# Kernel optimization log

Hardware: AMD Instinct MI355X
Metric: run time of the kernel (lower is better)

The kernel has to match this reference:

```python
import jax, jax.numpy as jnp
import numpy as np

B, I_LEN, Q_LEN, H = 256, 256, 64, 512
MID, G, FLAT_OUT = 512, 1, 1024


def setup_inputs() -> dict:
    key = jax.random.key(0)
    ks = jax.random.split(key, 20)
    s = lambda k, sh: jax.random.normal(k, sh, dtype=jnp.float32) * 0.02
    inp = {
        'i_batch': jax.random.normal(ks[0], (B, I_LEN, H), dtype=jnp.float32),
        'q_batch': jax.random.normal(ks[1], (B, Q_LEN, H), dtype=jnp.float32),
        'i_mask': jax.random.bernoulli(ks[2], 0.1, (B, 1, 1, I_LEN)),
        'q_mask': jax.random.bernoulli(ks[3], 0.1, (B, 1, 1, Q_LEN)),
        # l_flatten (applied to i_feat) params
        'lf_w1': s(ks[4], (H, MID)), 'lf_b1': jnp.zeros((MID,), jnp.float32),
        'lf_w2': s(ks[5], (MID, G)), 'lf_b2': jnp.zeros((G,), jnp.float32),
        'lf_wm': s(ks[6], (H * G, FLAT_OUT)), 'lf_bm': jnp.zeros((FLAT_OUT,), jnp.float32),
        # i_flatten (applied to l_feat) params
        'if_w1': s(ks[7], (H, MID)), 'if_b1': jnp.zeros((MID,), jnp.float32),
        'if_w2': s(ks[8], (MID, G)), 'if_b2': jnp.zeros((G,), jnp.float32),
        'if_wm': s(ks[9], (H * G, FLAT_OUT)), 'if_bm': jnp.zeros((FLAT_OUT,), jnp.float32),
        # fh_h: Linear(1024, 512)
        'fh_w': s(ks[10], (FLAT_OUT, 512)), 'fh_b': jnp.zeros((512,), jnp.float32),
    }
    return inp


def _qkv_attention(query, key, value, mask):
    # query [B,Lq,H], key/value [B,Lk,H], mask [B,1,1,Lk] (True = pad)
    d_k = query.shape[-1]
    scores = jnp.einsum('bqh,bkh->bqk', query, key) / jnp.sqrt(jnp.asarray(d_k, query.dtype))
    scores = jnp.where(mask[:, 0], jnp.asarray(-65504.0, scores.dtype), scores)
    p_attn = jax.nn.softmax(scores, axis=-1)
    return jnp.einsum('bqk,bkh->bqh', p_attn, value)


def _att_flat(x, x_mask, w1, b1, w2, b2, wm, bm):
    # x [B,L,H], x_mask [B,1,1,L]
    att = jnp.maximum(x @ w1 + b1, 0.0) @ w2 + b2           # [B,L,G]
    att = jnp.where(x_mask[:, 0, 0, :, None], -1e9, att)
    att = jax.nn.softmax(att, axis=1)
    pooled = jnp.einsum('blg,blh->bgh', att, x).reshape(x.shape[0], -1)  # [B,G*H]
    return pooled @ wm + bm, att[..., 0]                    # att.squeeze() with G=1


def reference(i_batch, q_batch, i_mask, q_mask,
              lf_w1, lf_b1, lf_w2, lf_b2, lf_wm, lf_bm,
              if_w1, if_b1, if_w2, if_b2, if_wm, if_bm,
              fh_w, fh_b):
    i_feat = _qkv_attention(i_batch, q_batch, q_batch, q_mask)   # [B,I_LEN,H]
    i_feat, i_weight = _att_flat(i_feat, i_mask, lf_w1, lf_b1, lf_w2, lf_b2, lf_wm, lf_bm)
    l_feat = _qkv_attention(q_batch, i_batch, i_batch, i_mask)   # [B,Q_LEN,H]
    l_feat, _ = _att_flat(l_feat, q_mask, if_w1, if_b1, if_w2, if_b2, if_wm, if_bm)
    out = (l_feat + i_feat) @ fh_w + fh_b                        # [B,512]
    return out, i_weight
```

## Files before the change

kernel.cpp:

```cpp
#include <hip/hip_runtime.h>
#include <math.h>


#define SCALE 0.04419417382415922f

typedef __attribute__((ext_vector_type(8))) short short8;
typedef __attribute__((ext_vector_type(4))) float floatx4;

__device__ __forceinline__ unsigned short f2bf(float x) {
  unsigned u = __float_as_uint(x);
  unsigned r = u + 0x7FFFu + ((u >> 16) & 1u);
  return (unsigned short)(r >> 16);
}
__device__ __forceinline__ float bf2f(unsigned short h) {
  return __uint_as_float(((unsigned)h) << 16);
}
__device__ __forceinline__ unsigned pk2(float a, float b) {
  return (unsigned)f2bf(a) | ((unsigned)f2bf(b) << 16);
}

__device__ __forceinline__ float wave_max(float v) {
#pragma unroll
  for (int o = 32; o > 0; o >>= 1) v = fmaxf(v, __shfl_xor(v, o, 64));
  return v;
}
__device__ __forceinline__ float wave_sum(float v) {
#pragma unroll
  for (int o = 32; o > 0; o >>= 1) v += __shfl_xor(v, o, 64);
  return v;
}

#define GLD_LDS16(gptr, lptr)                                             \
  __builtin_amdgcn_global_load_lds(                                       \
      (const __attribute__((address_space(1))) void*)(gptr),              \
      (__attribute__((address_space(3))) void*)(lptr), 16, 0, 0)

__global__ __launch_bounds__(256) void k_prep(
    const float* __restrict__ ib, const float* __restrict__ qb,
    const float* __restrict__ lf_w1, const float* __restrict__ if_w1,
    const float* __restrict__ lf_wm, const float* __restrict__ if_wm,
    const float* __restrict__ fh_w, unsigned short* __restrict__ ibT,
    unsigned short* __restrict__ qb_bf, unsigned short* __restrict__ w1t_lf,
    unsigned short* __restrict__ w1t_if, unsigned short* __restrict__ wcat_t,
    unsigned short* __restrict__ fh_wt) {
  __shared__ __align__(16) char smem[64 * 65 * 4];
  const int idx = blockIdx.x, t = threadIdx.x;

  if (idx < 512) {
    float(*T)[65] = (float(*)[65])smem;
    const float* src;
    unsigned short* dst;
    int N, ds, koff, k0, n0;
    if (idx < 64) {
      src = lf_w1; dst = w1t_lf; N = 512; ds = 512; koff = 0;
      k0 = (idx & 7) * 64; n0 = (idx >> 3) * 64;
    } else if (idx < 128) {
      int l = idx - 64;
      src = if_w1; dst = w1t_if; N = 512; ds = 512; koff = 0;
      k0 = (l & 7) * 64; n0 = (l >> 3) * 64;
    } else if (idx < 256) {
      int l = idx - 128;
      src = lf_wm; dst = wcat_t; N = 1024; ds = 1024; koff = 0;
      k0 = (l & 7) * 64; n0 = (l >> 3) * 64;
    } else if (idx < 384) {
      int l = idx - 256;
      src = if_wm; dst = wcat_t; N = 1024; ds = 1024; koff = 512;
      k0 = (l & 7) * 64; n0 = (l >> 3) * 64;
    } else {
      int l = idx - 384;
      src = fh_w; dst = fh_wt; N = 512; ds = 1024; koff = 0;
      k0 = (l & 15) * 64; n0 = (l >> 4) * 64;
    }
#pragma unroll
    for (int i = 0; i < 16; i++) {
      int e = t + i * 256, r = e >> 6, c = e & 63;
      T[r][c] = src[(size_t)(k0 + r) * N + n0 + c];
    }
    __syncthreads();
#pragma unroll
    for (int i = 0; i < 8; i++) {
      int e = t + i * 256, r = e >> 5, c2 = (e & 31) * 2;
      *(unsigned*)&dst[(size_t)(n0 + r) * ds + koff + k0 + c2] =
          pk2(T[c2][r], T[c2 + 1][r]);
    }
  } else if (idx < 4608) {
    int j = idx - 512;
    int b = j >> 4, tok0 = ((j >> 2) & 3) * 64, h0 = (j & 3) * 128;
    unsigned short* Tb = (unsigned short*)smem;
    const float* src = ib + ((size_t)b * 256 + tok0) * 512 + h0;
#pragma unroll
    for (int i = 0; i < 8; i++) {
      int e = t + i * 256, tok = e >> 5, h4 = (e & 31) * 4;
      float4 v = *(const float4*)&src[(size_t)tok * 512 + h4];
      uint2 p;
      p.x = pk2(v.x, v.y);
      p.y = pk2(v.z, v.w);
      int col = ((((h4 >> 3) ^ (tok >> 3)) & 15) << 3) | (h4 & 7);
      *(uint2*)&Tb[tok * 128 + col] = p;
    }
    __syncthreads();
    unsigned short* dT = ibT + ((size_t)b * 512 + h0) * 256 + tok0;
#pragma unroll
    for (int i = 0; i < 4; i++) {
      int e = t + i * 256, h = e >> 3, tc = (e & 7) * 8;
      int hg = h >> 3, ho = h & 7;
      unsigned y[8];
#pragma unroll
      for (int k = 0; k < 8; k++) {
        int r = tc + k;
        y[k] = Tb[r * 128 + (((hg ^ (r >> 3)) & 15) << 3) + ho];
      }
      uint4 v;
      v.x = y[0] | (y[1] << 16);
      v.y = y[2] | (y[3] << 16);
      v.z = y[4] | (y[5] << 16);
      v.w = y[6] | (y[7] << 16);
      *(uint4*)&dT[(size_t)h * 256 + tc] = v;
    }
  } else {
    int j = idx - 4608;
    const float4* src = (const float4*)(qb + (size_t)j * 4096);
    uint2* dst = (uint2*)(qb_bf + (size_t)j * 4096);
#pragma unroll
    for (int i = 0; i < 4; i++) {
      int e = t + i * 256;
      float4 v = src[e];
      uint2 p;
      p.x = pk2(v.x, v.y);
      p.y = pk2(v.z, v.w);
      dst[e] = p;
    }
  }
}

__global__ __launch_bounds__(256) void k_scores_f(
    const float* __restrict__ ib, const unsigned short* __restrict__ qbf,
    const int* __restrict__ imask, const int* __restrict__ qmask,
    unsigned short* __restrict__ P1, unsigned short* __restrict__ P2,
    float* __restrict__ psum) {
  __shared__ unsigned short As[64 * 64];
  __shared__ unsigned short Bs[128 * 64];
  __shared__ __align__(16) unsigned short X[128 * 72];
  const int b = blockIdx.y, ic = blockIdx.x, i0 = ic * 128;
  const int t = threadIdx.x, w = t >> 6, lane = t & 63, c = lane & 15, qq = lane >> 4;

  floatx4 acc[4][2];
#pragma unroll
  for (int ti = 0; ti < 4; ti++)
#pragma unroll
    for (int tj = 0; tj < 2; tj++) acc[ti][tj] = (floatx4){0.f, 0.f, 0.f, 0.f};

  for (int k0 = 0; k0 < 512; k0 += 64) {
#pragma unroll
    for (int i = 0; i < 2; i++) {
      int s = i * 256 + t, row = s >> 3, src = (s & 7) ^ (row & 7);
      GLD_LDS16(qbf + ((size_t)b * 64 + row) * 512 + k0 + src * 8,
                &As[(i * 256 + w * 64) * 8]);
    }
#pragma unroll
    for (int i = 0; i < 8; i++) {
      int s = i * 256 + t, row = s >> 4, c4 = s & 15;
      float4 v = *(const float4*)&ib[((size_t)b * 256 + i0 + row) * 512 + k0 + c4 * 4];
      int gs = (c4 >> 1) ^ (row & 7), sub = c4 & 1;
      uint2 p;
      p.x = pk2(v.x, v.y);
      p.y = pk2(v.z, v.w);
      *(uint2*)&Bs[row * 64 + gs * 8 + sub * 4] = p;
    }
    __syncthreads();
#pragma unroll
    for (int kk = 0; kk < 2; kk++) {
      short8 a[4], bb[2];
#pragma unroll
      for (int ti = 0; ti < 4; ti++)
        a[ti] = *(const short8*)&As[(ti * 16 + c) * 64 + ((kk * 4 + qq) ^ (c & 7)) * 8];
#pragma unroll
      for (int tj = 0; tj < 2; tj++)
        bb[tj] = *(const short8*)&Bs[(w * 32 + tj * 16 + c) * 64 + ((kk * 4 + qq) ^ (c & 7)) * 8];
#pragma unroll
      for (int ti = 0; ti < 4; ti++)
#pragma unroll
        for (int tj = 0; tj < 2; tj++)
          acc[ti][tj] = __builtin_amdgcn_mfma_f32_16x16x32_bf16(a[ti], bb[tj], acc[ti][tj], 0, 0, 0);
    }
    __syncthreads();
  }

  const int il0 = w * 32 + c;
  int imsk0 = imask[b * 256 + i0 + il0];
  int imsk1 = imask[b * 256 + i0 + il0 + 16];
  int qm[4][4];
#pragma unroll
  for (int ti = 0; ti < 4; ti++)
#pragma unroll
    for (int rr = 0; rr < 4; rr++) qm[ti][rr] = qmask[b * 64 + ti * 16 + qq * 4 + rr];

#pragma unroll
  for (int ti = 0; ti < 4; ti++)
#pragma unroll
    for (int rr = 0; rr < 4; rr++) {
      int qv = ti * 16 + qq * 4 + rr;
      float e0 = imsk0 ? 0.f : __expf(acc[ti][0][rr] * SCALE);
      float e1 = imsk1 ? 0.f : __expf(acc[ti][1][rr] * SCALE);
      X[qv * 136 + il0] = f2bf(e0);
      X[qv * 136 + il0 + 16] = f2bf(e1);
      float s = e0 + e1;
#pragma unroll
      for (int o = 1; o <= 8; o <<= 1) s += __shfl_xor(s, o, 64);
      if (c == 0) psum[((size_t)(b * 64 + qv)) * 8 + ic * 4 + w] = s;
    }
  __syncthreads();
#pragma unroll
  for (int i = 0; i < 4; i++) {
    int e2 = t + i * 256, qv = e2 >> 4, g = e2 & 15;
    *(uint4*)&P2[((size_t)b * 64 + qv) * 256 + i0 + g * 8] = *(const uint4*)&X[qv * 136 + g * 8];
  }
  __syncthreads();

#pragma unroll
  for (int tj = 0; tj < 2; tj++) {
    float ev[4][4];
    float s1 = 0.f;
#pragma unroll
    for (int ti = 0; ti < 4; ti++)
#pragma unroll
      for (int rr = 0; rr < 4; rr++) {
        ev[ti][rr] = qm[ti][rr] ? 0.f : __expf(acc[ti][tj][rr] * SCALE);
        s1 += ev[ti][rr];
      }
    s1 += __shfl_xor(s1, 16, 64);
    s1 += __shfl_xor(s1, 32, 64);
    float inv = 1.f / s1;
    int il = il0 + tj * 16;
#pragma unroll
    for (int ti = 0; ti < 4; ti++)
#pragma unroll
      for (int rr = 0; rr < 4; rr++)
        X[il * 72 + ti * 16 + qq * 4 + rr] = f2bf(ev[ti][rr] * inv);
  }
  __syncthreads();
#pragma unroll
  for (int i = 0; i < 4; i++) {
    int e2 = t + i * 256, il = e2 >> 3, g = e2 & 7;
    *(uint4*)&P1[((size_t)b * 256 + i0 + il) * 64 + g * 8] = *(const uint4*)&X[il * 72 + g * 8];
  }
}

__global__ __launch_bounds__(256) void k_av2(const unsigned short* __restrict__ P2,
                                             const unsigned short* __restrict__ ibT,
                                             const float* __restrict__ psum,
                                             unsigned short* __restrict__ lfeat) {
  __shared__ unsigned short As[64 * 64];
  __shared__ unsigned short Bs[128 * 64];
  const int b = blockIdx.y, n0 = blockIdx.x * 128;
  const int t = threadIdx.x, w = t >> 6, lane = t & 63, c = lane & 15, q = lane >> 4;
  const int wm = w >> 1, wn = w & 1;
  floatx4 acc[2][4];
#pragma unroll
  for (int ti = 0; ti < 2; ti++)
#pragma unroll
    for (int tj = 0; tj < 4; tj++) acc[ti][tj] = (floatx4){0.f, 0.f, 0.f, 0.f};

  for (int kc = 0; kc < 256; kc += 64) {
#pragma unroll
    for (int i = 0; i < 2; i++) {
      int s = i * 256 + t, row = s >> 3, src = (s & 7) ^ (row & 7);
      GLD_LDS16(P2 + ((size_t)b * 64 + row) * 256 + kc + src * 8, &As[(i * 256 + w * 64) * 8]);
    }
#pragma unroll
    for (int i = 0; i < 4; i++) {
      int s = i * 256 + t, row = s >> 3, src = (s & 7) ^ (row & 7);
      GLD_LDS16(ibT + ((size_t)b * 512 + n0 + row) * 256 + kc + src * 8,
                &Bs[(i * 256 + w * 64) * 8]);
    }
    __syncthreads();
#pragma unroll
    for (int kk = 0; kk < 2; kk++) {
      short8 a[2], bb[4];
#pragma unroll
      for (int ti = 0; ti < 2; ti++)
        a[ti] = *(const short8*)&As[(wm * 32 + ti * 16 + c) * 64 + ((kk * 4 + q) ^ (c & 7)) * 8];
#pragma unroll
      for (int tj = 0; tj < 4; tj++)
        bb[tj] = *(const short8*)&Bs[(wn * 64 + tj * 16 + c) * 64 + ((kk * 4 + q) ^ (c & 7)) * 8];
#pragma unroll
      for (int ti = 0; ti < 2; ti++)
#pragma unroll
        for (int tj = 0; tj < 4; tj++)
          acc[ti][tj] = __builtin_amdgcn_mfma_f32_16x16x32_bf16(a[ti], bb[tj], acc[ti][tj], 0, 0, 0);
    }
    __syncthreads();
  }
#pragma unroll
  for (int ti = 0; ti < 2; ti++)
#pragma unroll
    for (int rr = 0; rr < 4; rr++) {
      int m = wm * 32 + ti * 16 + q * 4 + rr;
      const float* ps = psum + ((size_t)(b * 64 + m)) * 8;
      float s = ps[0] + ps[1] + ps[2] + ps[3] + ps[4] + ps[5] + ps[6] + ps[7];
      float inv = 1.f / s;
      unsigned short* op = lfeat + ((size_t)b * 64 + m) * 512 + n0 + wn * 64;
#pragma unroll
      for (int tj = 0; tj < 4; tj++) op[tj * 16 + c] = f2bf(acc[ti][tj][rr] * inv);
    }
}

__global__ __launch_bounds__(256) void k_qbw1(const unsigned short* __restrict__ qbf,
                                              const unsigned short* __restrict__ W1t,
                                              unsigned short* __restrict__ qbW1T) {
  __shared__ unsigned short As[64 * 64];
  __shared__ unsigned short Bs[128 * 64];
  const int b = blockIdx.y, n0 = blockIdx.x * 128;
  const int t = threadIdx.x, w = t >> 6, lane = t & 63, c = lane & 15, q = lane >> 4;
  const int wm = w >> 1, wn = w & 1;
  floatx4 acc[2][4];
#pragma unroll
  for (int ti = 0; ti < 2; ti++)
#pragma unroll
    for (int tj = 0; tj < 4; tj++) acc[ti][tj] = (floatx4){0.f, 0.f, 0.f, 0.f};

  for (int k0 = 0; k0 < 512; k0 += 64) {
#pragma unroll
    for (int i = 0; i < 2; i++) {
      int s = i * 256 + t, row = s >> 3, src = (s & 7) ^ (row & 7);
      GLD_LDS16(qbf + ((size_t)b * 64 + row) * 512 + k0 + src * 8,
                &As[(i * 256 + w * 64) * 8]);
    }
#pragma unroll
    for (int i = 0; i < 4; i++) {
      int s = i * 256 + t, row = s >> 3, src = (s & 7) ^ (row & 7);
      GLD_LDS16(W1t + (size_t)(n0 + row) * 512 + k0 + src * 8,
                &Bs[(i * 256 + w * 64) * 8]);
    }
    __syncthreads();
#pragma unroll
    for (int kk = 0; kk < 2; kk++) {
      short8 a[2], bb[4];
#pragma unroll
      for (int ti = 0; ti < 2; ti++)
        a[ti] = *(const short8*)&As[(wm * 32 + ti * 16 + c) * 64 + ((kk * 4 + q) ^ (c & 7)) * 8];
#pragma unroll
      for (int tj = 0; tj < 4; tj++)
        bb[tj] = *(const short8*)&Bs[(wn * 64 + tj * 16 + c) * 64 + ((kk * 4 + q) ^ (c & 7)) * 8];
#pragma unroll
      for (int ti = 0; ti < 2; ti++)
#pragma unroll
        for (int tj = 0; tj < 4; tj++)
          acc[ti][tj] = __builtin_amdgcn_mfma_f32_16x16x32_bf16(a[ti], bb[tj], acc[ti][tj], 0, 0, 0);
    }
    __syncthreads();
  }
#pragma unroll
  for (int ti = 0; ti < 2; ti++)
#pragma unroll
    for (int tj = 0; tj < 4; tj++) {
      int n = n0 + wn * 64 + tj * 16 + c;
      int m = wm * 32 + ti * 16 + q * 4;
      uint2 p;
      p.x = pk2(acc[ti][tj][0], acc[ti][tj][1]);
      p.y = pk2(acc[ti][tj][2], acc[ti][tj][3]);
      *(uint2*)&qbW1T[((size_t)b * 512 + n) * 64 + m] = p;
    }
}

__global__ __launch_bounds__(256) void k_logits_i64(
    const unsigned short* __restrict__ P1, const unsigned short* __restrict__ qbW1T,
    const float* __restrict__ b1, const float* __restrict__ w2,
    float* __restrict__ outp) {
  __shared__ unsigned short As[128 * 64];
  __shared__ unsigned short Bs[128 * 64];
  __shared__ float red[2][128];
  const int b = blockIdx.y;
  const int mt = blockIdx.x & 1, nc = blockIdx.x >> 1;
  const int m0 = mt * 128, n0 = nc * 128;
  const int t = threadIdx.x, w = t >> 6, lane = t & 63, c = lane & 15, q = lane >> 4;
  const int wm = w >> 1, wn = w & 1;

#pragma unroll
  for (int i = 0; i < 4; i++) {
    int s = i * 256 + t, row = s >> 3, src = (s & 7) ^ (row & 7);
    GLD_LDS16(P1 + ((size_t)b * 256 + m0 + row) * 64 + src * 8, &As[(i * 256 + w * 64) * 8]);
  }
#pragma unroll
  for (int i = 0; i < 4; i++) {
    int s = i * 256 + t, row = s >> 3, src = (s & 7) ^ (row & 7);
    GLD_LDS16(qbW1T + ((size_t)b * 512 + n0 + row) * 64 + src * 8, &Bs[(i * 256 + w * 64) * 8]);
  }
  __syncthreads();
  floatx4 acc[4][4];
#pragma unroll
  for (int ti = 0; ti < 4; ti++)
#pragma unroll
    for (int tj = 0; tj < 4; tj++) acc[ti][tj] = (floatx4){0.f, 0.f, 0.f, 0.f};
#pragma unroll
  for (int kk = 0; kk < 2; kk++) {
    short8 a[4], bb[4];
#pragma unroll
    for (int ti = 0; ti < 4; ti++)
      a[ti] = *(const short8*)&As[(wm * 64 + ti * 16 + c) * 64 + ((kk * 4 + q) ^ (c & 7)) * 8];
#pragma unroll
    for (int tj = 0; tj < 4; tj++)
      bb[tj] = *(const short8*)&Bs[(wn * 64 + tj * 16 + c) * 64 + ((kk * 4 + q) ^ (c & 7)) * 8];
#pragma unroll
    for (int ti = 0; ti < 4; ti++)
#pragma unroll
      for (int tj = 0; tj < 4; tj++)
        acc[ti][tj] = __builtin_amdgcn_mfma_f32_16x16x32_bf16(a[ti], bb[tj], acc[ti][tj], 0, 0, 0);
  }

  float partial[4][4] = {};
#pragma unroll
  for (int tj = 0; tj < 4; tj++) {
    int n = n0 + wn * 64 + tj * 16 + c;
    float bia = b1[n], wwv = w2[n];
#pragma unroll
    for (int ti = 0; ti < 4; ti++)
#pragma unroll
      for (int r = 0; r < 4; r++)
        partial[ti][r] += fmaxf(acc[ti][tj][r] + bia, 0.f) * wwv;
  }
#pragma unroll
  for (int msk = 1; msk <= 8; msk <<= 1)
#pragma unroll
    for (int ti = 0; ti < 4; ti++)
#pragma unroll
      for (int r = 0; r < 4; r++)
        partial[ti][r] += __shfl_xor(partial[ti][r], msk, 64);
  if (c == 0) {
#pragma unroll
    for (int ti = 0; ti < 4; ti++)
#pragma unroll
      for (int r = 0; r < 4; r++)
        red[wn][wm * 64 + ti * 16 + q * 4 + r] = partial[ti][r];
  }
  __syncthreads();
  if (t < 128) outp[(size_t)nc * 65536 + b * 256 + m0 + t] = red[0][t] + red[1][t];
}

__global__ __launch_bounds__(256) void k_logits_part(
    const unsigned short* __restrict__ X, const unsigned short* __restrict__ W1t,
    const float* __restrict__ b1, const float* __restrict__ w2,
    float* __restrict__ outp, int M) {
  __shared__ unsigned short As[128 * 64];
  __shared__ unsigned short Bs[128 * 64];
  __shared__ float red[2][128];
  const int t = threadIdx.x, w = t >> 6, lane = t & 63;
  const int wm = w >> 1, wn = w & 1, c = lane & 15, q = lane >> 4;
  const int idx = blockIdx.x;
  const int m_tile = (idx & 7) + ((idx >> 5) << 3), nc = (idx >> 3) & 3;
  const int m0 = m_tile * 128, n0 = nc * 128;

  floatx4 acc[4][4];
#pragma unroll
  for (int ti = 0; ti < 4; ti++)
#pragma unroll
    for (int tj = 0; tj < 4; tj++) acc[ti][tj] = (floatx4){0.f, 0.f, 0.f, 0.f};

  for (int k0 = 0; k0 < 512; k0 += 64) {
#pragma unroll
    for (int it = 0; it < 4; it++) {
      int s = it * 256 + t, row = s >> 3, src = (s & 7) ^ (row & 7);
      GLD_LDS16(X + (size_t)(m0 + row) * 512 + k0 + src * 8, &As[(it * 256 + w * 64) * 8]);
      GLD_LDS16(W1t + (size_t)(n0 + row) * 512 + k0 + src * 8, &Bs[(it * 256 + w * 64) * 8]);
    }
    __syncthreads();
#pragma unroll
    for (int kk = 0; kk < 2; kk++) {
      short8 a[4], bb[4];
#pragma unroll
      for (int ti = 0; ti < 4; ti++)
        a[ti] = *(const short8*)&As[(wm * 64 + ti * 16 + c) * 64 + ((kk * 4 + q) ^ (c & 7)) * 8];
#pragma unroll
      for (int tj = 0; tj < 4; tj++)
        bb[tj] = *(const short8*)&Bs[(wn * 64 + tj * 16 + c) * 64 + ((kk * 4 + q) ^ (c & 7)) * 8];
#pragma unroll
      for (int ti = 0; ti < 4; ti++)
#pragma unroll
        for (int tj = 0; tj < 4; tj++)
          acc[ti][tj] = __builtin_amdgcn_mfma_f32_16x16x32_bf16(a[ti], bb[tj], acc[ti][tj], 0, 0, 0);
    }
    __syncthreads();
  }
  float partial[4][4] = {};
#pragma unroll
  for (int tj = 0; tj < 4; tj++) {
    int n = n0 + wn * 64 + tj * 16 + c;
    float bia = b1[n], wwv = w2[n];
#pragma unroll
    for (int ti = 0; ti < 4; ti++)
#pragma unroll
      for (int r = 0; r < 4; r++)
        partial[ti][r] += fmaxf(acc[ti][tj][r] + bia, 0.f) * wwv;
  }
#pragma unroll
  for (int msk = 1; msk <= 8; msk <<= 1)
#pragma unroll
    for (int ti = 0; ti < 4; ti++)
#pragma unroll
      for (int r = 0; r < 4; r++)
        partial[ti][r] += __shfl_xor(partial[ti][r], msk, 64);
  if (c == 0) {
#pragma unroll
    for (int ti = 0; ti < 4; ti++)
#pragma unroll
      for (int r = 0; r < 4; r++)
        red[wn][wm * 64 + ti * 16 + q * 4 + r] = partial[ti][r];
  }
  __syncthreads();
  if (t < 128) outp[(size_t)nc * M + m0 + t] = red[0][t] + red[1][t];
}

__global__ __launch_bounds__(256) void k_final_i(const float* __restrict__ lp,
                                                 const int* __restrict__ imask,
                                                 const unsigned short* __restrict__ P1,
                                                 const unsigned short* __restrict__ qbf,
                                                 float* __restrict__ iw_out,
                                                 unsigned short* __restrict__ pooled) {
  __shared__ float red4[4];
  __shared__ float ar[256];
  __shared__ float red[4][64];
  __shared__ float vsm[64];
  const int b = blockIdx.x, t = threadIdx.x;
  const int i = b * 256 + t;
  float x = lp[i] + lp[65536 + i] + lp[131072 + i] + lp[196608 + i];
  float v = imask[i] ? -1e9f : x;
  float wmx = wave_max(v);
  if ((t & 63) == 0) red4[t >> 6] = wmx;
  __syncthreads();
  float mx = fmaxf(fmaxf(red4[0], red4[1]), fmaxf(red4[2], red4[3]));
  __syncthreads();
  float e = __expf(v - mx);
  float ws = wave_sum(e);
  if ((t & 63) == 0) red4[t >> 6] = ws;
  __syncthreads();
  float s = red4[0] + red4[1] + red4[2] + red4[3];
  float p = e / s;
  iw_out[i] = p;
  ar[t] = p;
  __syncthreads();
  const int part = t >> 6, lane = t & 63;
  const unsigned short* Pb = P1 + ((size_t)b * 256 + part * 64) * 64 + lane;
  float s0 = 0.f, s1 = 0.f;
#pragma unroll 8
  for (int ii = 0; ii < 64; ii += 2) {
    s0 += ar[part * 64 + ii] * bf2f(Pb[(size_t)ii * 64]);
    s1 += ar[part * 64 + ii + 1] * bf2f(Pb[(size_t)(ii + 1) * 64]);
  }
  red[part][lane] = s0 + s1;
  __syncthreads();
  if (t < 64) vsm[t] = red[0][t] + red[1][t] + red[2][t] + red[3][t];
  __syncthreads();
  float a0 = 0.f, a1 = 0.f;
  const unsigned short* Xb = qbf + (size_t)b * 64 * 512 + 2 * t;
#pragma unroll 4
  for (int l = 0; l < 64; l++) {
    unsigned u = *(const unsigned*)&Xb[(size_t)l * 512];
    float a = vsm[l];
    a0 += a * bf2f((unsigned short)(u & 0xffff));
    a1 += a * bf2f((unsigned short)(u >> 16));
  }
  *(unsigned*)&pooled[(size_t)b * 1024 + 2 * t] = pk2(a0, a1);
}

__global__ __launch_bounds__(256) void k_final_l(const float* __restrict__ lp,
                                                 const int* __restrict__ qmask,
                                                 const unsigned short* __restrict__ lfeat,
                                                 unsigned short* __restrict__ pooled) {
  __shared__ float ar[64];
  const int b = blockIdx.x, t = threadIdx.x;
  if (t < 64) {
    const int i = b * 64 + t;
    float x = lp[i] + lp[16384 + i] + lp[32768 + i] + lp[49152 + i];
    float v = qmask[i] ? -1e9f : x;
    float mx = wave_max(v);
    float e = __expf(v - mx);
    float s = wave_sum(e);
    ar[t] = e / s;
  }
  __syncthreads();
  float a0 = 0.f, a1 = 0.f;
  const unsigned short* Xb = lfeat + (size_t)b * 64 * 512 + 2 * t;
#pragma unroll 4
  for (int l = 0; l < 64; l++) {
    unsigned u = *(const unsigned*)&Xb[(size_t)l * 512];
    float a = ar[l];
    a0 += a * bf2f((unsigned short)(u & 0xffff));
    a1 += a * bf2f((unsigned short)(u >> 16));
  }
  *(unsigned*)&pooled[(size_t)b * 1024 + 512 + 2 * t] = pk2(a0, a1);
}

__global__ __launch_bounds__(256) void k_egemm(const unsigned short* __restrict__ X,
                                               const unsigned short* __restrict__ Wt,
                                               const float* __restrict__ biasA,
                                               const float* __restrict__ biasB,
                                               float* __restrict__ outf,
                                               unsigned short* __restrict__ outbf,
                                               int N, int K) {
  __shared__ unsigned short As[64 * 64];
  __shared__ unsigned short Bs[64 * 64];
  const int n0 = blockIdx.x * 64, m0 = blockIdx.y * 64;
  const int t = threadIdx.x, w = t >> 6, lane = t & 63, c = lane & 15, q = lane >> 4;
  const int wm = w >> 1, wn = w & 1;
  floatx4 acc[2][2];
#pragma unroll
  for (int ti = 0; ti < 2; ti++)
#pragma unroll
    for (int tj = 0; tj < 2; tj++) acc[ti][tj] = (floatx4){0.f, 0.f, 0.f, 0.f};

  for (int k0 = 0; k0 < K; k0 += 64) {
#pragma unroll
    for (int i = 0; i < 2; i++) {
      int s = i * 256 + t, row = s >> 3, src = (s & 7) ^ (row & 7);
      GLD_LDS16(X + (size_t)(m0 + row) * K + k0 + src * 8, &As[(i * 256 + w * 64) * 8]);
      GLD_LDS16(Wt + (size_t)(n0 + row) * K + k0 + src * 8, &Bs[(i * 256 + w * 64) * 8]);
    }
    __syncthreads();
#pragma unroll
    for (int kk = 0; kk < 2; kk++) {
      short8 a[2], bb[2];
#pragma unroll
      for (int ti = 0; ti < 2; ti++)
        a[ti] = *(const short8*)&As[(wm * 32 + ti * 16 + c) * 64 + ((kk * 4 + q) ^ (c & 7)) * 8];
#pragma unroll
      for (int tj = 0; tj < 2; tj++)
        bb[tj] = *(const short8*)&Bs[(wn * 32 + tj * 16 + c) * 64 + ((kk * 4 + q) ^ (c & 7)) * 8];
#pragma unroll
      for (int ti = 0; ti < 2; ti++)
#pragma unroll
        for (int tj = 0; tj < 2; tj++)
          acc[ti][tj] = __builtin_amdgcn_mfma_f32_16x16x32_bf16(a[ti], bb[tj], acc[ti][tj], 0, 0, 0);
    }
    __syncthreads();
  }
#pragma unroll
  for (int tj = 0; tj < 2; tj++) {
    int n = n0 + wn * 32 + tj * 16 + c;
    float bias = biasA[n] + (biasB ? biasB[n] : 0.f);
#pragma unroll
    for (int ti = 0; ti < 2; ti++)
#pragma unroll
      for (int rr = 0; rr < 4; rr++) {
        int m = m0 + wm * 32 + ti * 16 + q * 4 + rr;
        float v = acc[ti][tj][rr] + bias;
        if (outbf) outbf[(size_t)m * N + n] = f2bf(v);
        else outf[(size_t)m * N + n] = v;
      }
  }
}

extern "C" void kernel_launch(void* const* d_in, const int* in_sizes, int n_in,
                              void* d_out, int out_size, void* d_ws, size_t ws_size,
                              hipStream_t stream) {
  const float* ib = (const float*)d_in[0];
  const float* qb = (const float*)d_in[1];
  const int* imask = (const int*)d_in[2];
  const int* qmask = (const int*)d_in[3];
  const float* lf_w1 = (const float*)d_in[4];
  const float* lf_b1 = (const float*)d_in[5];
  const float* lf_w2 = (const float*)d_in[6];
  const float* lf_wm = (const float*)d_in[8];
  const float* lf_bm = (const float*)d_in[9];
  const float* if_w1 = (const float*)d_in[10];
  const float* if_b1 = (const float*)d_in[11];
  const float* if_w2 = (const float*)d_in[12];
  const float* if_wm = (const float*)d_in[14];
  const float* if_bm = (const float*)d_in[15];
  const float* fh_w = (const float*)d_in[16];
  const float* fh_b = (const float*)d_in[17];
  float* out = (float*)d_out;

  float* lp_i = (float*)d_ws;
  float* lp_l = lp_i + 262144;
  float* att_i = lp_l + 65536;
  float* att_l = att_i + 65536;
  float* psum = att_l + 16384;
  unsigned short* P1 = (unsigned short*)(psum + 131072);
  unsigned short* P2 = P1 + 4194304;
  unsigned short* lfeat = P2 + 4194304;
  unsigned short* qb_bf = lfeat + 33554432;
  unsigned short* qbW1T = qb_bf + 8388608;
  unsigned short* ibT = qbW1T + 8388608;
  unsigned short* w1t_lf = ibT + 33554432;
  unsigned short* w1t_if = w1t_lf + 262144;
  unsigned short* wcat_t = w1t_if + 262144;
  unsigned short* fh_wt = wcat_t + 1048576;
  unsigned short* pooled_bf = fh_wt + 524288;
  unsigned short* F_bf = pooled_bf + 262144;

  k_prep<<<6656, 256, 0, stream>>>(ib, qb, lf_w1, if_w1, lf_wm, if_wm, fh_w,
                                   ibT, qb_bf, w1t_lf, w1t_if, wcat_t, fh_wt);

  k_scores_f<<<dim3(2, 256), 256, 0, stream>>>(ib, qb_bf, imask, qmask, P1, P2, psum);
  k_av2<<<dim3(4, 256), 256, 0, stream>>>(P2, ibT, psum, lfeat);
  k_qbw1<<<dim3(4, 256), 256, 0, stream>>>(qb_bf, w1t_lf, qbW1T);
  k_logits_i64<<<dim3(8, 256), 256, 0, stream>>>(P1, qbW1T, lf_b1, lf_w2, lp_i);
  k_logits_part<<<512, 256, 0, stream>>>(lfeat, w1t_if, if_b1, if_w2, lp_l, 16384);
  k_final_i<<<256, 256, 0, stream>>>(lp_i, imask, P1, qb_bf, out + 131072, pooled_bf);
  k_final_l<<<256, 256, 0, stream>>>(lp_l, qmask, lfeat, pooled_bf);

  k_egemm<<<dim3(16, 4), 256, 0, stream>>>(pooled_bf, wcat_t, lf_bm, if_bm,
                                           nullptr, F_bf, 1024, 1024);
  k_egemm<<<dim3(8, 4), 256, 0, stream>>>(F_bf, fh_wt, fh_b, nullptr,
                                          out, nullptr, 512, 1024);
}
```

Before: 416.2 us.

## Fuse i_batch bf16 transpose into k_av2 B-tile loading

After: 381.3 us. 1.09x faster.

```diff
diff --git a/kernel.cpp b/kernel.cpp
--- a/kernel.cpp
+++ b/kernel.cpp
@@ -36,10 +36,9 @@
       (__attribute__((address_space(3))) void*)(lptr), 16, 0, 0)
 
 __global__ __launch_bounds__(256) void k_prep(
-    const float* __restrict__ ib, const float* __restrict__ qb,
-    const float* __restrict__ lf_w1, const float* __restrict__ if_w1,
-    const float* __restrict__ lf_wm, const float* __restrict__ if_wm,
-    const float* __restrict__ fh_w, unsigned short* __restrict__ ibT,
+    const float* __restrict__ qb, const float* __restrict__ lf_w1,
+    const float* __restrict__ if_w1, const float* __restrict__ lf_wm,
+    const float* __restrict__ if_wm, const float* __restrict__ fh_w,
     unsigned short* __restrict__ qb_bf, unsigned short* __restrict__ w1t_lf,
     unsigned short* __restrict__ w1t_if, unsigned short* __restrict__ wcat_t,
     unsigned short* __restrict__ fh_wt) {
@@ -83,42 +82,8 @@
       *(unsigned*)&dst[(size_t)(n0 + r) * ds + koff + k0 + c2] =
           pk2(T[c2][r], T[c2 + 1][r]);
     }
-  } else if (idx < 4608) {
+  } else {
     int j = idx - 512;
-    int b = j >> 4, tok0 = ((j >> 2) & 3) * 64, h0 = (j & 3) * 128;
-    unsigned short* Tb = (unsigned short*)smem;
-    const float* src = ib + ((size_t)b * 256 + tok0) * 512 + h0;
-#pragma unroll
-    for (int i = 0; i < 8; i++) {
-      int e = t + i * 256, tok = e >> 5, h4 = (e & 31) * 4;
-      float4 v = *(const float4*)&src[(size_t)tok * 512 + h4];
-      uint2 p;
-      p.x = pk2(v.x, v.y);
-      p.y = pk2(v.z, v.w);
-      int col = ((((h4 >> 3) ^ (tok >> 3)) & 15) << 3) | (h4 & 7);
-      *(uint2*)&Tb[tok * 128 + col] = p;
-    }
-    __syncthreads();
-    unsigned short* dT = ibT + ((size_t)b * 512 + h0) * 256 + tok0;
-#pragma unroll
-    for (int i = 0; i < 4; i++) {
-      int e = t + i * 256, h = e >> 3, tc = (e & 7) * 8;
-      int hg = h >> 3, ho = h & 7;
-      unsigned y[8];
-#pragma unroll
-      for (int k = 0; k < 8; k++) {
-        int r = tc + k;
-        y[k] = Tb[r * 128 + (((hg ^ (r >> 3)) & 15) << 3) + ho];
-      }
-      uint4 v;
-      v.x = y[0] | (y[1] << 16);
-      v.y = y[2] | (y[3] << 16);
-      v.z = y[4] | (y[5] << 16);
-      v.w = y[6] | (y[7] << 16);
-      *(uint4*)&dT[(size_t)h * 256 + tc] = v;
-    }
-  } else {
-    int j = idx - 4608;
     const float4* src = (const float4*)(qb + (size_t)j * 4096);
     uint2* dst = (uint2*)(qb_bf + (size_t)j * 4096);
 #pragma unroll
@@ -247,11 +212,12 @@
 }
 
 __global__ __launch_bounds__(256) void k_av2(const unsigned short* __restrict__ P2,
-                                             const unsigned short* __restrict__ ibT,
+                                             const float* __restrict__ ib,
                                              const float* __restrict__ psum,
                                              unsigned short* __restrict__ lfeat) {
   __shared__ unsigned short As[64 * 64];
   __shared__ unsigned short Bs[128 * 64];
+  __shared__ __align__(16) unsigned short Tb[64 * 128];
   const int b = blockIdx.y, n0 = blockIdx.x * 128;
   const int t = threadIdx.x, w = t >> 6, lane = t & 63, c = lane & 15, q = lane >> 4;
   const int wm = w >> 1, wn = w & 1;
@@ -268,10 +234,32 @@
       GLD_LDS16(P2 + ((size_t)b * 64 + row) * 256 + kc + src * 8, &As[(i * 256 + w * 64) * 8]);
     }
 #pragma unroll
+    for (int i = 0; i < 8; i++) {
+      int e = i * 256 + t, tok = e >> 5, h4 = (e & 31) * 4;
+      float4 v = *(const float4*)&ib[((size_t)b * 256 + kc + tok) * 512 + n0 + h4];
+      uint2 p;
+      p.x = pk2(v.x, v.y);
+      p.y = pk2(v.z, v.w);
+      int col = ((((h4 >> 3) ^ (tok >> 3)) & 15) << 3) | (h4 & 7);
+      *(uint2*)&Tb[tok * 128 + col] = p;
+    }
+    __syncthreads();
+#pragma unroll
     for (int i = 0; i < 4; i++) {
-      int s = i * 256 + t, row = s >> 3, src = (s & 7) ^ (row & 7);
-      GLD_LDS16(ibT + ((size_t)b * 512 + n0 + row) * 256 + kc + src * 8,
-                &Bs[(i * 256 + w * 64) * 8]);
+      int e = i * 256 + t, h = e >> 3, tc = (e & 7) * 8;
+      int hg = h >> 3, ho = h & 7;
+      unsigned y[8];
+#pragma unroll
+      for (int k = 0; k < 8; k++) {
+        int r = tc + k;
+        y[k] = Tb[r * 128 + (((hg ^ (r >> 3)) & 15) << 3) + ho];
+      }
+      uint4 vv;
+      vv.x = y[0] | (y[1] << 16);
+      vv.y = y[2] | (y[3] << 16);
+      vv.z = y[4] | (y[5] << 16);
+      vv.w = y[6] | (y[7] << 16);
+      *(uint4*)&Bs[h * 64 + (((tc >> 3) ^ (h & 7)) << 3)] = vv;
     }
     __syncthreads();
 #pragma unroll
@@ -680,19 +668,19 @@
   unsigned short* lfeat = P2 + 4194304;
   unsigned short* qb_bf = lfeat + 33554432;
   unsigned short* qbW1T = qb_bf + 8388608;
-  unsigned short* ibT = qbW1T + 8388608;
-  unsigned short* w1t_lf = ibT + 33554432;
+  unsigned short* ibT_unused = qbW1T + 8388608;
+  unsigned short* w1t_lf = ibT_unused + 33554432;
   unsigned short* w1t_if = w1t_lf + 262144;
   unsigned short* wcat_t = w1t_if + 262144;
   unsigned short* fh_wt = wcat_t + 1048576;
   unsigned short* pooled_bf = fh_wt + 524288;
   unsigned short* F_bf = pooled_bf + 262144;
 
-  k_prep<<<6656, 256, 0, stream>>>(ib, qb, lf_w1, if_w1, lf_wm, if_wm, fh_w,
-                                   ibT, qb_bf, w1t_lf, w1t_if, wcat_t, fh_wt);
+  k_prep<<<2560, 256, 0, stream>>>(qb, lf_w1, if_w1, lf_wm, if_wm, fh_w,
+                                   qb_bf, w1t_lf, w1t_if, wcat_t, fh_wt);
 
   k_scores_f<<<dim3(2, 256), 256, 0, stream>>>(ib, qb_bf, imask, qmask, P1, P2, psum);
-  k_av2<<<dim3(4, 256), 256, 0, stream>>>(P2, ibT, psum, lfeat);
+  k_av2<<<dim3(4, 256), 256, 0, stream>>>(P2, ib, psum, lfeat);
   k_qbw1<<<dim3(4, 256), 256, 0, stream>>>(qb_bf, w1t_lf, qbW1T);
   k_logits_i64<<<dim3(8, 256), 256, 0, stream>>>(P1, qbW1T, lf_b1, lf_w2, lp_i);
   k_logits_part<<<512, 256, 0, stream>>>(lfeat, w1t_if, if_b1, if_w2, lp_l, 16384);
```
